# Kernel optimization log

Measured on AMD Instinct MI355X. Metric: run time of the kernel, lower is better.

Reference implementation:

```python
import math
import jax, jax.numpy as jnp
import numpy as np

# CoordinateDescentRouter defaults (lucidrains/CoLT5-attention)
N_ITERS, EPS, EPS_INIT, EPS_DECAY, FETCH_K_RATIO = 20, 0.03, 4.0, 0.7, 9.0 / 8.0

B, N, D, G, H, DH, NQ, NKV = 2, 4096, 1024, 2, 16, 64, 1024, 1024
DIM_INNER = H * DH  # 1024


def coor_descent(s, k):
    # s: (b, g, n). Differentiable top-k relaxation via coordinate descent.
    logk = math.log(k)
    eps_sched = [max(EPS_INIT * EPS_DECAY ** i, EPS) for i in range(N_ITERS + 1)]
    b = -s
    a = jnp.zeros_like(s[..., :1])
    for ce in eps_sched[:-1]:
        sb = (s + b) / ce
        a = ce * (logk - jax.scipy.special.logsumexp(sb, axis=-1, keepdims=True))
        b = -jax.nn.relu(s + a)
    return jnp.exp((s + a + b) / eps_sched[-1])


def route(x, routing_tokens, num_tokens):
    # x: (b,n,d), routing_tokens: (g,d) -> indices (b,g,nt), scores (b,g,nt), routed (b,g,nt,d)
    bsz, n, _ = x.shape
    k_cd = min(int(num_tokens * FETCH_K_RATIO), n)
    sim = jnp.einsum('bnd,gd->bgn', x, routing_tokens)
    scores = coor_descent(sim, k_cd)
    scores, idx = jax.lax.top_k(scores, num_tokens)
    # straight-through: forward value 1.0, gradient flows through coor_descent scores
    scores = scores + jax.lax.stop_gradient(1.0 - scores)
    routed = x[jnp.arange(bsz)[:, None, None], idx]
    return idx, scores, routed


def rmsnorm(t, gamma):
    # t: (b,g,n,d); F.normalize over feature dim * sqrt(d) * gamma (g,d)
    norm = jnp.sqrt(jnp.sum(t * t, axis=-1, keepdims=True))
    return t / jnp.maximum(norm, 1e-12) * math.sqrt(t.shape[-1]) * gamma[None, :, None, :]


def grouped_attention(queries, kvs, v_scale, o_scale, gamma_q, gamma_c, wq, wkv, wo, null_kv):
    bsz, g, nq, d = queries.shape
    h, dh = null_kv.shape[2], null_kv.shape[-1]
    qn = rmsnorm(queries, gamma_q)
    cn = rmsnorm(kvs, gamma_c)
    # grouped 1x1 conv == per-group linear; within-group output channel order is (h, dh)
    q = jnp.einsum('bgnd,ged->bgne', qn, wq)
    kv = jnp.einsum('bgnd,ged->bgne', cn, wkv)
    k, v = jnp.split(kv, 2, axis=-1)

    def to_heads(t):
        return t.reshape(bsz, g, t.shape[2], h, dh).transpose(0, 1, 3, 2, 4)  # (b,g,h,n,dh)

    q, k, v = map(to_heads, (q, k, v))
    v = v * v_scale  # (b,g,1,nkv,1) broadcast, applied before null kv concat
    nk = jnp.broadcast_to(null_kv[0][None], (bsz,) + null_kv[0].shape)
    nv = jnp.broadcast_to(null_kv[1][None], (bsz,) + null_kv[1].shape)
    k = jnp.concatenate([nk, k], axis=-2)
    v = jnp.concatenate([nv, v], axis=-2)
    sim = jnp.einsum('bghnd,bghmd->bghnm', q * dh ** -0.5, k)
    attn = jax.nn.softmax(sim, axis=-1)
    o = jnp.einsum('bghnm,bghmd->bghnd', attn, v)
    o = o.transpose(0, 1, 3, 2, 4).reshape(bsz, g, nq, h * dh)
    o = jnp.einsum('bgne,gde->bgnd', o, wo)
    return o * o_scale


def setup_inputs() -> dict:
    key = jax.random.key(0)
    ks = jax.random.split(key, 8)
    inv = 1.0 / math.sqrt(D)
    return {
        'x': jax.random.normal(ks[0], (B, N, D), jnp.float32),
        'rt_q': jax.random.normal(ks[1], (G, D), jnp.float32),
        'rt_kv': jax.random.normal(ks[2], (G, D), jnp.float32),
        'gamma_q': jnp.ones((G, D), jnp.float32),
        'gamma_c': jnp.ones((G, D), jnp.float32),
        'wq': jax.random.normal(ks[3], (G, DIM_INNER, D), jnp.float32) * inv,
        'wkv': jax.random.normal(ks[4], (G, 2 * DIM_INNER, D), jnp.float32) * inv,
        'wo': jax.random.normal(ks[5], (G, D, DIM_INNER), jnp.float32) * inv,
        'null_kv': jax.random.normal(ks[6], (2, G, H, 1, DH), jnp.float32),
        'null_token': jax.random.normal(ks[7], (1, 1, D), jnp.float32),
        'num_routed_queries': NQ,
        'num_routed_key_values': NKV,
    }


def reference(x, rt_q, rt_kv, gamma_q, gamma_c, wq, wkv, wo, null_kv, null_token,
              num_routed_queries, num_routed_key_values):
    bsz, n, d = x.shape
    q_idx, q_scores, queries = route(x, rt_q, num_routed_queries)
    _, kv_scores, key_values = route(x, rt_kv, num_routed_key_values)
    v_scale = kv_scores[:, :, None, :, None]  # (b,g,1,nkv,1)
    o_scale = q_scores[..., None]             # (b,g,nq,1)
    attn_out = grouped_attention(queries, key_values, v_scale, o_scale,
                                 gamma_q, gamma_c, wq, wkv, wo, null_kv)
    # scatter routed outputs back, averaging over experts that picked each token
    flat_idx = q_idx.reshape(bsz, -1)                 # (b, g*nq)
    flat_out = attn_out.reshape(bsz, -1, d)           # (b, g*nq, d)
    bidx = jnp.arange(bsz)[:, None]
    summed = jnp.zeros_like(x).at[bidx, flat_idx].add(flat_out)
    counts = jnp.zeros((bsz, n), x.dtype).at[bidx, flat_idx].add(1.0)
    not_routed = (counts == 0.0)[..., None]
    summed = jnp.where(not_routed, 0.0, summed)
    out = summed / jnp.maximum(counts[..., None], 1e-5)
    out = jnp.where(not_routed, null_token, out)
    return out
```

## Files before the change

### kernel.cpp

```cpp
#include <hip/hip_runtime.h>

typedef __attribute__((ext_vector_type(8))) short short8;
typedef __attribute__((ext_vector_type(4))) short short4v;
typedef __attribute__((ext_vector_type(4))) float f32x4;

#define B_ 2
#define N_ 4096
#define D_ 1024
#define G_ 2
#define H_ 16
#define DH_ 64
#define NSLOT 1088
#define LOGK 7.0492548412558374f
#define ATTN_SCALE 0.18033688011112043f
#define FIXED_M 32.0f

#define BAR() __builtin_amdgcn_s_barrier()
#define WAITV4 asm volatile("s_waitcnt vmcnt(4)" ::: "memory")
#define WAITV0 asm volatile("s_waitcnt vmcnt(0)" ::: "memory")
#define GLDS(src, dst) __builtin_amdgcn_global_load_lds( \
    (const __attribute__((address_space(1))) void*)(src), \
    (__attribute__((address_space(3))) void*)(dst), 16, 0, 0)

__device__ __forceinline__ float bf2f(short s) {
  return __uint_as_float(((unsigned)(unsigned short)s) << 16);
}
__device__ __forceinline__ short f2bf(float f) {
  unsigned u = __float_as_uint(f);
  u = (u + 0x7FFFu + ((u >> 16) & 1u)) >> 16;
  return (short)u;
}
__device__ __forceinline__ short f2bf_trunc(float f) {
  return (short)(__float_as_uint(f) >> 16);
}

__global__ __launch_bounds__(256) void prep_kernel(
    const float* __restrict__ wq, const float* __restrict__ wkv,
    const float* __restrict__ wo, short* __restrict__ dq,
    short* __restrict__ dkv, short* __restrict__ dwo,
    const float* __restrict__ x, const float* __restrict__ rtq,
    const float* __restrict__ rtkv, float* __restrict__ sim,
    const float* __restrict__ null_kv, short* __restrict__ kb_,
    short* __restrict__ vb_)
{
  int bid = blockIdx.x;
  if (bid < 8192) {
    int i = bid * 256 + threadIdx.x;
    const float* src; short* dst;
    if (i < 524288) { src = wq; dst = dq; }
    else if (i < 1572864) { src = wkv; dst = dkv; i -= 524288; }
    else { src = wo; dst = dwo; i -= 1572864; }
    f32x4 v = ((const f32x4*)src)[i];
    short4v o;
#pragma unroll
    for (int e = 0; e < 4; ++e) o[e] = f2bf(v[e]);
    ((short4v*)dst)[i] = o;
  } else if (bid < 10240) {
    int wid = threadIdx.x >> 6, lane = threadIdx.x & 63;
    int row = (bid - 8192) * 4 + wid;
    int b = row >> 12, n = row & (N_ - 1);
    const float* xr = x + (size_t)row * D_;
    float a0 = 0.f, a1 = 0.f, a2 = 0.f, a3 = 0.f;
#pragma unroll
    for (int c = 0; c < 4; ++c) {
      int d = c * 256 + lane * 4;
      f32x4 xv = *(const f32x4*)(xr + d);
      f32x4 r0 = *(const f32x4*)(rtq + d);
      f32x4 r1 = *(const f32x4*)(rtq + D_ + d);
      f32x4 r2 = *(const f32x4*)(rtkv + d);
      f32x4 r3 = *(const f32x4*)(rtkv + D_ + d);
#pragma unroll
      for (int e = 0; e < 4; ++e) {
        a0 += xv[e] * r0[e];
        a1 += xv[e] * r1[e];
        a2 += xv[e] * r2[e];
        a3 += xv[e] * r3[e];
      }
    }
#pragma unroll
    for (int o = 32; o; o >>= 1) {
      a0 += __shfl_xor(a0, o); a1 += __shfl_xor(a1, o);
      a2 += __shfl_xor(a2, o); a3 += __shfl_xor(a3, o);
    }
    if (lane == 0) {
      sim[((size_t)(b)*G_ + 0) * N_ + n] = a0;
      sim[((size_t)(b)*G_ + 1) * N_ + n] = a1;
      sim[((size_t)(B_ + b)*G_ + 0) * N_ + n] = a2;
      sim[((size_t)(B_ + b)*G_ + 1) * N_ + n] = a3;
    }
  } else {
    int bgh = (bid - 10240) * 4 + (threadIdx.x >> 6);
    int g = (bgh >> 4) & 1, h = bgh & 15;
    int t = threadIdx.x & 63;
    float kvk = null_kv[((size_t)(0 * G_ + g) * H_ + h) * DH_ + t];
    float kvv = null_kv[((size_t)(1 * G_ + g) * H_ + h) * DH_ + t];
    kb_[((size_t)bgh * NSLOT + 1024) * DH_ + t] = f2bf(kvk);
    vb_[((size_t)bgh * DH_ + t) * NSLOT + 1024] = f2bf(kvv);
  }
}

__global__ __launch_bounds__(1024) void coor_topk(
    const float* __restrict__ sim, int* __restrict__ idxout, int* __restrict__ inv)
{
  __shared__ float rbuf[16];
  __shared__ float res;
  __shared__ unsigned keys[N_];
  __shared__ int scanbuf[16];

  int r = blockIdx.x >> 2, b = (blockIdx.x >> 1) & 1, g = blockIdx.x & 1;
  const float* srow = sim + ((size_t)blockIdx.x << 12);
  int tid = threadIdx.x, lane = tid & 63, wid = tid >> 6;

  float sv[4];
#pragma unroll
  for (int j = 0; j < 4; ++j) sv[j] = srow[tid * 4 + j];

  float a = 0.f;
  double epsd = 4.0;
  for (int it = 0; it < 20; ++it) {
    float eps = (float)fmax(epsd, 0.03);
    epsd *= 0.7;
    float sb[4]; float lmax = -INFINITY;
#pragma unroll
    for (int j = 0; j < 4; ++j) {
      float bb = (it == 0) ? (-sv[j]) : (-fmaxf(sv[j] + a, 0.f));
      sb[j] = (sv[j] + bb) / eps;
      lmax = fmaxf(lmax, sb[j]);
    }
#pragma unroll
    for (int o = 32; o; o >>= 1) lmax = fmaxf(lmax, __shfl_xor(lmax, o));
    if (lane == 0) rbuf[wid] = lmax;
    __syncthreads();
    if (tid < 64) {
      float m = (tid < 16) ? rbuf[tid] : -INFINITY;
#pragma unroll
      for (int o = 8; o; o >>= 1) m = fmaxf(m, __shfl_xor(m, o));
      if (tid == 0) res = m;
    }
    __syncthreads();
    float mx = res;
    float lsum = 0.f;
#pragma unroll
    for (int j = 0; j < 4; ++j) lsum += expf(sb[j] - mx);
#pragma unroll
    for (int o = 32; o; o >>= 1) lsum += __shfl_xor(lsum, o);
    if (lane == 0) rbuf[wid] = lsum;
    __syncthreads();
    if (tid < 64) {
      float s = (tid < 16) ? rbuf[tid] : 0.f;
#pragma unroll
      for (int o = 8; o; o >>= 1) s += __shfl_xor(s, o);
      if (tid == 0) res = logf(s) + mx;
    }
    __syncthreads();
    float lse = res;
    a = eps * (LOGK - lse);
  }
  __syncthreads();

  unsigned kb[4]; int c1 = 0;
#pragma unroll
  for (int j = 0; j < 4; ++j) {
    float sc = expf(fminf(sv[j] + a, 0.f) / 0.03f);
    kb[j] = __float_as_uint(sc);
    keys[tid * 4 + j] = kb[j];
    c1 += (kb[j] == 0x3F800000u);
  }
#pragma unroll
  for (int o = 32; o; o >>= 1) c1 += __shfl_xor(c1, o);
  if (lane == 0) scanbuf[wid] = c1;
  __syncthreads();
  int c1tot = 0;
  for (int i = 0; i < 16; ++i) c1tot += scanbuf[i];
  __syncthreads();

  int flag[4];
  if (c1tot >= 1024) {
#pragma unroll
    for (int j = 0; j < 4; ++j) flag[j] = (kb[j] == 0x3F800000u);
  } else {
#pragma unroll
    for (int j = 0; j < 4; ++j) {
      unsigned kn = kb[j]; int n = tid * 4 + j; int rank = 0;
      for (int m = 0; m < N_; ++m) {
        unsigned km = keys[m];
        rank += (km > kn) || (km == kn && m < n);
      }
      flag[j] = (rank < 1024);
    }
  }

  int cnt = flag[0] + flag[1] + flag[2] + flag[3];
  int inc = cnt;
#pragma unroll
  for (int o = 1; o < 64; o <<= 1) {
    int tt = __shfl_up(inc, o);
    if (lane >= o) inc += tt;
  }
  if (lane == 63) scanbuf[wid] = inc;
  __syncthreads();
  int off = 0;
  for (int w = 0; w < wid; ++w) off += scanbuf[w];
  int pos = off + inc - cnt;
  int* op = idxout + ((size_t)blockIdx.x << 10);
  int* ip = inv + ((size_t)(b * G_ + g) << 12);
#pragma unroll
  for (int j = 0; j < 4; ++j) {
    if (flag[j]) {
      if (pos < 1024) {
        int n = tid * 4 + j;
        op[pos] = n;
        if (r == 0) ip[n] = pos;
      }
      pos++;
    }
  }
}

__global__ __launch_bounds__(256) void gather_rms(
    const float* __restrict__ x, const int* __restrict__ idx,
    const float* __restrict__ gamma_q, const float* __restrict__ gamma_c,
    short* __restrict__ qn, short* __restrict__ cn)
{
  __shared__ float rb[4];
  __shared__ float tot;
  int id = blockIdx.x;
  int r = id >> 12, rem = id & 4095;
  int g = (rem >> 10) & 1;
  int b = rem >> 11;
  int tok = idx[id];
  int t = threadIdx.x;
  const float* xr = x + ((size_t)b * N_ + tok) * D_;
  f32x4 v = *(const f32x4*)(xr + t * 4);
  float ss = v[0]*v[0] + v[1]*v[1] + v[2]*v[2] + v[3]*v[3];
#pragma unroll
  for (int o = 32; o; o >>= 1) ss += __shfl_xor(ss, o);
  if ((t & 63) == 0) rb[t >> 6] = ss;
  __syncthreads();
  if (t == 0) tot = rb[0] + rb[1] + rb[2] + rb[3];
  __syncthreads();
  float scale = 32.0f / fmaxf(sqrtf(tot), 1e-12f);
  const float* gm = (r ? gamma_c : gamma_q) + g * D_;
  f32x4 gv = *(const f32x4*)(gm + t * 4);
  short* dst = (r ? cn : qn) + ((size_t)rem << 10) + t * 4;
  short4v ov;
#pragma unroll
  for (int e = 0; e < 4; ++e) ov[e] = f2bf(v[e] * scale * gv[e]);
  *(short4v*)dst = ov;
}

__global__ __launch_bounds__(256, 3) void gemm_qkv(
    const short* __restrict__ qn, const short* __restrict__ cn,
    const short* __restrict__ wqb, const short* __restrict__ wkvb,
    short* __restrict__ qout, short* __restrict__ kout, short* __restrict__ vout)
{
  __shared__ short As[8192];
  __shared__ short Bs[8192];
  int t = threadIdx.x, lane = t & 63, wid = t >> 6;
  int grp = lane >> 4, l15 = lane & 15;
  int wm = wid >> 1, wn = wid & 1;
  int lin = blockIdx.x + 8 * (blockIdx.y + 24 * blockIdx.z);
  int s = (lin & 7) * 96 + (lin >> 3);
  int bx = s & 7, ny = (s >> 3) % 24, bg = s / 192;
  bool isq = ny < 8;
  const short* A  = isq ? qn : cn;
  const short* Bw = isq ? wqb : wkvb;
  int NB = isq ? 1024 : 2048;
  int nbase = (isq ? ny : ny - 8) * 128;
  float oscale = isq ? ATTN_SCALE : 1.0f;
  int mbase = bx * 128;
  int g = bg & 1;
  const short* Ab = A + ((size_t)bg << 20);
  const short* Bp = Bw + ((size_t)g * NB + nbase) * 1024;

  f32x4 zero = {0.f, 0.f, 0.f, 0.f};
  f32x4 acc[4][4];
#pragma unroll
  for (int i = 0; i < 4; ++i)
#pragma unroll
    for (int j = 0; j < 4; ++j) acc[i][j] = zero;

  const short* apA[4]; const short* apB[4]; int dstoff[4];
#pragma unroll
  for (int c = 0; c < 4; ++c) {
    int u = c * 256 + t;
    int row = u >> 3, j = u & 7;
    int cu = (j ^ (row & 7)) << 3;
    apA[c] = Ab + ((size_t)(mbase + row) << 10) + cu;
    apB[c] = Bp + ((size_t)row << 10) + cu;
    dstoff[c] = c * 2048 + wid * 512;
  }

  for (int kb = 0; kb < 16; ++kb) {
    int ko = kb * 64;
    if (kb) __syncthreads();
#pragma unroll
    for (int c = 0; c < 4; ++c) {
      GLDS(apA[c] + ko, As + dstoff[c]);
      GLDS(apB[c] + ko, Bs + dstoff[c]);
    }
    WAITV0;
    __syncthreads();
    const char* Ac = (const char*)As;
    const char* Bc = (const char*)Bs;
#pragma unroll
    for (int kf = 0; kf < 2; ++kf) {
      short8 af[4], bf_[4];
#pragma unroll
      for (int mt = 0; mt < 4; ++mt) {
        int ra = wm * 64 + mt * 16 + l15;
        af[mt] = *(const short8*)(Ac + ra * 128 + (((grp << 4) + (kf << 6)) ^ ((ra & 7) << 4)));
      }
#pragma unroll
      for (int nt = 0; nt < 4; ++nt) {
        int rb = wn * 64 + nt * 16 + l15;
        bf_[nt] = *(const short8*)(Bc + rb * 128 + (((grp << 4) + (kf << 6)) ^ ((rb & 7) << 4)));
      }
      __builtin_amdgcn_s_setprio(1);
#pragma unroll
      for (int mt = 0; mt < 4; ++mt)
#pragma unroll
        for (int nt = 0; nt < 4; ++nt)
          acc[mt][nt] = __builtin_amdgcn_mfma_f32_16x16x32_bf16(af[mt], bf_[nt], acc[mt][nt], 0, 0, 0);
      __builtin_amdgcn_s_setprio(0);
    }
  }

#pragma unroll
  for (int mt = 0; mt < 4; ++mt)
#pragma unroll
    for (int nt = 0; nt < 4; ++nt) {
      int n = nbase + wn*64 + nt*16 + l15;
#pragma unroll
      for (int rr = 0; rr < 4; ++rr) {
        int m = mbase + wm*64 + mt*16 + grp*4 + rr;
        float v = acc[mt][nt][rr] * oscale;
        if (isq) {
          qout[((size_t)bg * 1024 + m) * 1024 + n] = f2bf(v);
        } else {
          if (n < 1024) {
            kout[(((size_t)bg * H_ + (n >> 6)) * NSLOT + m) * DH_ + (n & 63)] = f2bf(v);
          } else {
            int e = n - 1024;
            vout[(((size_t)bg * H_ + (e >> 6)) * DH_ + (e & 63)) * NSLOT + m] = f2bf(v);
          }
        }
      }
    }
}

__global__ __launch_bounds__(256, 3) void gemm_wo(
    const short* __restrict__ A, const short* __restrict__ Bw,
    short* __restrict__ out0, short* __restrict__ out1)
{
  __shared__ short As[8192];
  __shared__ short Bs[8192];
  int t = threadIdx.x, lane = t & 63, wid = t >> 6;
  int grp = lane >> 4, l15 = lane & 15;
  int wm = wid >> 1, wn = wid & 1;
  int lin = blockIdx.x + 8 * (blockIdx.y + 8 * blockIdx.z);
  int s = (lin & 7) * 64 + (lin >> 3);
  int mbase = (s & 7) * 128, nbase = ((s >> 3) & 7) * 128;
  int z = s >> 6, bg = z >> 1, sp = z & 1, g = bg & 1;
  short* out = sp ? out1 : out0;
  const short* Ab = A + ((size_t)bg << 20);
  const short* Bp = Bw + ((size_t)g * 1024 + nbase) * 1024;

  f32x4 zero = {0.f, 0.f, 0.f, 0.f};
  f32x4 acc[4][4];
#pragma unroll
  for (int i = 0; i < 4; ++i)
#pragma unroll
    for (int j = 0; j < 4; ++j) acc[i][j] = zero;

  const short* apA[4]; const short* apB[4]; int dstoff[4];
#pragma unroll
  for (int c = 0; c < 4; ++c) {
    int u = c * 256 + t;
    int row = u >> 3, j = u & 7;
    int cu = (j ^ (row & 7)) << 3;
    apA[c] = Ab + ((size_t)(mbase + row) << 10) + cu;
    apB[c] = Bp + ((size_t)row << 10) + cu;
    dstoff[c] = c * 2048 + wid * 512;
  }

  int kb0 = sp * 8;
  for (int kk = 0; kk < 8; ++kk) {
    int ko = (kb0 + kk) * 64;
    if (kk) __syncthreads();
#pragma unroll
    for (int c = 0; c < 4; ++c) {
      GLDS(apA[c] + ko, As + dstoff[c]);
      GLDS(apB[c] + ko, Bs + dstoff[c]);
    }
    WAITV0;
    __syncthreads();
    const char* Ac = (const char*)As;
    const char* Bc = (const char*)Bs;
#pragma unroll
    for (int kf = 0; kf < 2; ++kf) {
      short8 af[4], bf_[4];
#pragma unroll
      for (int mt = 0; mt < 4; ++mt) {
        int ra = wm * 64 + mt * 16 + l15;
        af[mt] = *(const short8*)(Ac + ra * 128 + (((grp << 4) + (kf << 6)) ^ ((ra & 7) << 4)));
      }
#pragma unroll
      for (int nt = 0; nt < 4; ++nt) {
        int rb = wn * 64 + nt * 16 + l15;
        bf_[nt] = *(const short8*)(Bc + rb * 128 + (((grp << 4) + (kf << 6)) ^ ((rb & 7) << 4)));
      }
      __builtin_amdgcn_s_setprio(1);
#pragma unroll
      for (int mt = 0; mt < 4; ++mt)
#pragma unroll
        for (int nt = 0; nt < 4; ++nt)
          acc[mt][nt] = __builtin_amdgcn_mfma_f32_16x16x32_bf16(af[mt], bf_[nt], acc[mt][nt], 0, 0, 0);
      __builtin_amdgcn_s_setprio(0);
    }
  }

#pragma unroll
  for (int mt = 0; mt < 4; ++mt)
#pragma unroll
    for (int nt = 0; nt < 4; ++nt) {
      int n = nbase + wn*64 + nt*16 + l15;
#pragma unroll
      for (int rr = 0; rr < 4; ++rr) {
        int m = mbase + wm*64 + mt*16 + grp*4 + rr;
        out[((size_t)bg * 1024 + m) * 1024 + n] = f2bf(acc[mt][nt][rr]);
      }
    }
}

__global__ __launch_bounds__(256, 3) void attn_kernel(
    const short* __restrict__ q, const short* __restrict__ k,
    const short* __restrict__ vT, short* __restrict__ o0,
    short* __restrict__ o1, float* __restrict__ ml)
{
  __shared__ short Ks[2][4096];
  __shared__ short Vs[2][4096];
  __shared__ short Ps[4][32 * 72];
  int bgh = blockIdx.x, qb = blockIdx.y, sp = blockIdx.z;
  int bg = bgh >> 4, h = bgh & 15;
  int wid = threadIdx.x >> 6, lane = threadIdx.x & 63;
  int l15 = lane & 15, grp = lane >> 4;
  int qbase = qb * 128 + wid * 32;
  short* Pw = &Ps[wid][0];

  short8 bq[2][2];
#pragma unroll
  for (int qh = 0; qh < 2; ++qh) {
    const short* qp = q + ((size_t)bg * 1024 + qbase + qh * 16 + l15) * 1024 + h * 64 + (grp << 3);
    bq[qh][0] = *(const short8*)qp;
    bq[qh][1] = *(const short8*)(qp + 32);
  }
  short8 ones8;
  short ov = (l15 == 0) ? (short)0x3F80 : (short)0;
#pragma unroll
  for (int e = 0; e < 8; ++e) ones8[e] = ov;

  int u0 = wid * 128 + lane, u1 = u0 + 64;
  int r0 = u0 >> 3, j0 = u0 & 7, r1 = u1 >> 3, j1 = u1 & 7;
  const short* kbase = k + (size_t)bgh * NSLOT * DH_;
  const short* vbase = vT + (size_t)bgh * DH_ * NSLOT;
  const short* kss0 = kbase + r0 * 64 + ((j0 ^ (r0 & 7)) << 3);
  const short* kss1 = kbase + r1 * 64 + ((j1 ^ (r1 & 7)) << 3);
  const short* vss0 = vbase + (size_t)r0 * NSLOT + ((j0 ^ (r0 & 7)) << 3);
  const short* vss1 = vbase + (size_t)r1 * NSLOT + ((j1 ^ (r1 & 7)) << 3);

  f32x4 zero = {0.f, 0.f, 0.f, 0.f};
  f32x4 minit = {-FIXED_M, -FIXED_M, -FIXED_M, -FIXED_M};
  f32x4 oacc[2][4], lacc[2];
#pragma unroll
  for (int qh = 0; qh < 2; ++qh) {
    lacc[qh] = zero;
#pragma unroll
    for (int dt = 0; dt < 4; ++dt) oacc[qh][dt] = zero;
  }

  auto STAGE = [&](int tile, int p) {
    size_t ko = (size_t)tile * 4096;
    size_t vo = (size_t)tile * 64;
    short* kd = &Ks[p][0] + wid * 1024;
    short* vd = &Vs[p][0] + wid * 1024;
    GLDS(kss0 + ko, kd);
    GLDS(kss1 + ko, kd + 512);
    GLDS(vss0 + vo, vd);
    GLDS(vss1 + vo, vd + 512);
  };

  auto PROCESS = [&](int tile, int p) {
    const char* Kc = (const char*)&Ks[p][0];
    const char* Vc = (const char*)&Vs[p][0];
    f32x4 sacc[2][4];
#pragma unroll
    for (int qh = 0; qh < 2; ++qh)
#pragma unroll
      for (int kt = 0; kt < 4; ++kt) sacc[qh][kt] = minit;
#pragma unroll
    for (int kf = 0; kf < 2; ++kf) {
      short8 ka[4];
#pragma unroll
      for (int kt = 0; kt < 4; ++kt) {
        int ra = kt * 16 + l15;
        ka[kt] = *(const short8*)(Kc + ra * 128 + (((grp + 4 * kf) ^ (ra & 7)) << 4));
      }
      __builtin_amdgcn_s_setprio(1);
#pragma unroll
      for (int kt = 0; kt < 4; ++kt)
#pragma unroll
        for (int qh = 0; qh < 2; ++qh)
          sacc[qh][kt] = __builtin_amdgcn_mfma_f32_16x16x32_bf16(ka[kt], bq[qh][kf], sacc[qh][kt], 0, 0, 0);
      __builtin_amdgcn_s_setprio(0);
    }
    if (tile == 16) {
#pragma unroll
      for (int qh = 0; qh < 2; ++qh)
#pragma unroll
        for (int kt = 0; kt < 4; ++kt)
#pragma unroll
          for (int rr = 0; rr < 4; ++rr)
            if ((kt * 16 + (grp << 2) + rr) != 0) sacc[qh][kt][rr] = -INFINITY;
    }
#pragma unroll
    for (int qh = 0; qh < 2; ++qh)
#pragma unroll
      for (int kt = 0; kt < 4; ++kt) {
        short4v pk;
#pragma unroll
        for (int rr = 0; rr < 4; ++rr) pk[rr] = f2bf_trunc(exp2f(sacc[qh][kt][rr]));
        *(short4v*)(Pw + (qh * 16 + l15) * 72 + kt * 16 + (grp << 2)) = pk;
      }
#pragma unroll
    for (int ks = 0; ks < 2; ++ks) {
      short8 pa[2];
#pragma unroll
      for (int qh = 0; qh < 2; ++qh)
        pa[qh] = *(const short8*)((const char*)Pw + (qh * 16 + l15) * 144 + grp * 16 + ks * 64);
      __builtin_amdgcn_s_setprio(1);
#pragma unroll
      for (int dt = 0; dt < 4; ++dt) {
        int ra = dt * 16 + l15;
        short8 vbf = *(const short8*)(Vc + ra * 128 + (((grp + 4 * ks) ^ (ra & 7)) << 4));
#pragma unroll
        for (int qh = 0; qh < 2; ++qh)
          oacc[qh][dt] = __builtin_amdgcn_mfma_f32_16x16x32_bf16(pa[qh], vbf, oacc[qh][dt], 0, 0, 0);
      }
#pragma unroll
      for (int qh = 0; qh < 2; ++qh)
        lacc[qh] = __builtin_amdgcn_mfma_f32_16x16x32_bf16(pa[qh], ones8, lacc[qh], 0, 0, 0);
      __builtin_amdgcn_s_setprio(0);
    }
  };

  int t0 = sp ? 8 : 0, t1 = sp ? 17 : 8;
  STAGE(t0, 0);
  STAGE(t0 + 1, 1);
  WAITV4;
  BAR();
  for (int tile = t0; tile < t1; ++tile) {
    int p = (tile - t0) & 1;
    PROCESS(tile, p);
    if (tile + 1 < t1) {
      BAR();
      if (tile + 2 < t1) { STAGE(tile + 2, p); WAITV4; }
      else               { WAITV0; }
      BAR();
    }
  }

  if (l15 == 0) {
#pragma unroll
    for (int qh = 0; qh < 2; ++qh)
#pragma unroll
      for (int rr = 0; rr < 4; ++rr)
        ml[(size_t)(sp * 64 + bgh) * 1024 + qbase + qh * 16 + (grp << 2) + rr] = lacc[qh][rr];
  }
#pragma unroll
  for (int qh = 0; qh < 2; ++qh)
#pragma unroll
    for (int dt = 0; dt < 4; ++dt)
#pragma unroll
      for (int rr = 0; rr < 4; ++rr) {
        int qq = qh * 16 + (grp << 2) + rr;
        int dh = dt * 16 + l15;
        if (sp == 0)
          o0[((size_t)bg * 1024 + qbase + qq) * 1024 + h * 64 + dh] = f2bf(oacc[qh][dt][rr]);
        else
          o1[((size_t)bgh * 1024 + qbase + qq) * 64 + dh] = f2bf(oacc[qh][dt][rr]);
      }
}

__global__ __launch_bounds__(256) void attn_merge(
    short* __restrict__ obuf, const short* __restrict__ op1,
    const float* __restrict__ ml)
{
  int id = blockIdx.x;
  int bgh = id >> 4, qc = id & 15;
  int bg = bgh >> 4, h = bgh & 15;
  int t = threadIdx.x;
  int qq = t >> 2, c = t & 3;
  int qrow = qc * 64 + qq;
  float l0 = ml[(size_t)bgh * 1024 + qrow];
  float l1 = ml[(size_t)(64 + bgh) * 1024 + qrow];
  float w = 1.0f / (l0 + l1);
  size_t loc0 = ((size_t)bg * 1024 + qrow) * 1024 + h * 64 + c * 16;
  size_t loc1 = ((size_t)bgh * 1024 + qrow) * 64 + c * 16;
  short8 a0 = *(const short8*)(obuf + loc0);
  short8 a1 = *(const short8*)(obuf + loc0 + 8);
  short8 b0 = *(const short8*)(op1 + loc1);
  short8 b1 = *(const short8*)(op1 + loc1 + 8);
  short8 r0, r1;
#pragma unroll
  for (int e = 0; e < 8; ++e) {
    r0[e] = f2bf((bf2f(a0[e]) + bf2f(b0[e])) * w);
    r1[e] = f2bf((bf2f(a1[e]) + bf2f(b1[e])) * w);
  }
  *(short8*)(obuf + loc0) = r0;
  *(short8*)(obuf + loc0 + 8) = r1;
}

__global__ __launch_bounds__(256) void finalize_kernel(
    const short* __restrict__ wo0, const short* __restrict__ wo1,
    const int* __restrict__ inv, const float* __restrict__ null_token,
    float* __restrict__ outp)
{
  int id = blockIdx.x;
  int b = id >> 12, n = id & (N_ - 1);
  int s0 = inv[((size_t)(b * G_ + 0) << 12) + n];
  int s1 = inv[((size_t)(b * G_ + 1) << 12) + n];
  int t = threadIdx.x;
  float* dst = outp + (size_t)id * D_ + t * 4;
  if (s0 < 0 && s1 < 0) {
    *(f32x4*)dst = *(const f32x4*)(null_token + t * 4);
  } else {
    f32x4 sum = {0.f, 0.f, 0.f, 0.f};
    float cnt = 0.f;
    if (s0 >= 0) {
      size_t loc = (((size_t)(b * G_ + 0) * 1024 + s0) << 10) + t * 4;
      short4v v = *(const short4v*)(wo0 + loc);
      short4v v2 = *(const short4v*)(wo1 + loc);
#pragma unroll
      for (int e = 0; e < 4; ++e) sum[e] += bf2f(v[e]) + bf2f(v2[e]);
      cnt += 1.f;
    }
    if (s1 >= 0) {
      size_t loc = (((size_t)(b * G_ + 1) * 1024 + s1) << 10) + t * 4;
      short4v v = *(const short4v*)(wo0 + loc);
      short4v v2 = *(const short4v*)(wo1 + loc);
#pragma unroll
      for (int e = 0; e < 4; ++e) sum[e] += bf2f(v[e]) + bf2f(v2[e]);
      cnt += 1.f;
    }
    f32x4 rv;
#pragma unroll
    for (int e = 0; e < 4; ++e) rv[e] = sum[e] / cnt;
    *(f32x4*)dst = rv;
  }
}

extern "C" void kernel_launch(void* const* d_in, const int* in_sizes, int n_in,
                              void* d_out, int out_size, void* d_ws, size_t ws_size,
                              hipStream_t stream) {
  (void)in_sizes; (void)n_in; (void)out_size; (void)ws_size;
  const float* x        = (const float*)d_in[0];
  const float* rt_q     = (const float*)d_in[1];
  const float* rt_kv    = (const float*)d_in[2];
  const float* gamma_q  = (const float*)d_in[3];
  const float* gamma_c  = (const float*)d_in[4];
  const float* wq       = (const float*)d_in[5];
  const float* wkv      = (const float*)d_in[6];
  const float* wo       = (const float*)d_in[7];
  const float* null_kv  = (const float*)d_in[8];
  const float* null_tok = (const float*)d_in[9];
  float* outp = (float*)d_out;

  char* ws = (char*)d_ws;
  size_t off = 0;
  auto alloc = [&](size_t bytes) { char* p = ws + off; off += (bytes + 255) & ~(size_t)255; return p; };
  float* sim   = (float*)alloc((size_t)2 * B_ * G_ * N_ * 4);
  int*   idx   = (int*)  alloc((size_t)2 * B_ * G_ * 1024 * 4);
  int*   inv   = (int*)  alloc((size_t)B_ * G_ * N_ * 4);
  float* ml    = (float*)alloc((size_t)2 * 64 * 1024 * 4);
  short* qn    = (short*)alloc((size_t)B_ * G_ * 1024 * 1024 * 2);
  short* cn    = (short*)alloc((size_t)B_ * G_ * 1024 * 1024 * 2);
  short* qproj = (short*)alloc((size_t)B_ * G_ * 1024 * 1024 * 2);
  size_t kvbytes = (size_t)B_ * G_ * H_ * NSLOT * DH_ * 2;
  short* kbuf  = (short*)alloc(kvbytes);
  short* vbuf  = (short*)alloc(kvbytes);
  short* obuf  = (short*)alloc((size_t)B_ * G_ * 1024 * 1024 * 2);
  short* wobuf = (short*)alloc((size_t)B_ * G_ * 1024 * 1024 * 2);
  short* wo_bf = (short*)alloc((size_t)G_ * 1024 * 1024 * 2);
  short* wq_bf  = wobuf;
  short* wkv_bf = obuf;
  short* op1    = cn;
  short* wobuf2 = qproj;

  hipMemsetAsync(inv, 0xFF, (size_t)B_ * G_ * N_ * 4, stream);

  prep_kernel<<<10256, 256, 0, stream>>>(wq, wkv, wo, wq_bf, wkv_bf, wo_bf,
                                         x, rt_q, rt_kv, sim, null_kv, kbuf, vbuf);
  coor_topk<<<8, 1024, 0, stream>>>(sim, idx, inv);
  gather_rms<<<2 * B_ * G_ * 1024, 256, 0, stream>>>(x, idx, gamma_q, gamma_c, qn, cn);
  gemm_qkv<<<dim3(8, 24, B_ * G_), 256, 0, stream>>>(qn, cn, wq_bf, wkv_bf, qproj, kbuf, vbuf);
  attn_kernel<<<dim3(64, 8, 2), 256, 0, stream>>>(qproj, kbuf, vbuf, obuf, op1, ml);
  attn_merge<<<1024, 256, 0, stream>>>(obuf, op1, ml);
  gemm_wo<<<dim3(8, 8, 2 * B_ * G_), 256, 0, stream>>>(obuf, wo_bf, wobuf, wobuf2);
  finalize_kernel<<<B_ * N_, 256, 0, stream>>>(wobuf, wobuf2, inv, null_tok, outp);
}
```

Baseline: 169.7 us.

## Overlap weight bf16 conversion with top-k kernel and merge softmax reductions

Moves the fp32-to-bf16 weight conversion out of the prep kernel and into extra blocks of the coordinate-descent top-k kernel. The 8 serial top-k blocks then share the GPU with conversion work instead of running nearly alone. It also merges the max and sum reductions in each coordinate-descent iteration into one online log-sum-exp pass, removing two block barriers per iteration. The risks are that the 1024-thread conversion blocks may be scheduled ahead of the top-k blocks, and that the top-k blocks' large shared allocation now also applies to conversion blocks, which can limit occupancy.

```diff
diff --git a/kernel.cpp b/kernel.cpp
--- a/kernel.cpp
+++ b/kernel.cpp
@@ -35,29 +35,15 @@
 }
 
 __global__ __launch_bounds__(256) void prep_kernel(
-    const float* __restrict__ wq, const float* __restrict__ wkv,
-    const float* __restrict__ wo, short* __restrict__ dq,
-    short* __restrict__ dkv, short* __restrict__ dwo,
     const float* __restrict__ x, const float* __restrict__ rtq,
     const float* __restrict__ rtkv, float* __restrict__ sim,
     const float* __restrict__ null_kv, short* __restrict__ kb_,
     short* __restrict__ vb_)
 {
   int bid = blockIdx.x;
-  if (bid < 8192) {
-    int i = bid * 256 + threadIdx.x;
-    const float* src; short* dst;
-    if (i < 524288) { src = wq; dst = dq; }
-    else if (i < 1572864) { src = wkv; dst = dkv; i -= 524288; }
-    else { src = wo; dst = dwo; i -= 1572864; }
-    f32x4 v = ((const f32x4*)src)[i];
-    short4v o;
-#pragma unroll
-    for (int e = 0; e < 4; ++e) o[e] = f2bf(v[e]);
-    ((short4v*)dst)[i] = o;
-  } else if (bid < 10240) {
+  if (bid < 2048) {
     int wid = threadIdx.x >> 6, lane = threadIdx.x & 63;
-    int row = (bid - 8192) * 4 + wid;
+    int row = bid * 4 + wid;
     int b = row >> 12, n = row & (N_ - 1);
     const float* xr = x + (size_t)row * D_;
     float a0 = 0.f, a1 = 0.f, a2 = 0.f, a3 = 0.f;
@@ -89,7 +75,7 @@
       sim[((size_t)(B_ + b)*G_ + 1) * N_ + n] = a3;
     }
   } else {
-    int bgh = (bid - 10240) * 4 + (threadIdx.x >> 6);
+    int bgh = (bid - 2048) * 4 + (threadIdx.x >> 6);
     int g = (bgh >> 4) & 1, h = bgh & 15;
     int t = threadIdx.x & 63;
     float kvk = null_kv[((size_t)(0 * G_ + g) * H_ + h) * DH_ + t];
@@ -99,10 +85,32 @@
   }
 }
 
-__global__ __launch_bounds__(1024) void coor_topk(
-    const float* __restrict__ sim, int* __restrict__ idxout, int* __restrict__ inv)
+__global__ __launch_bounds__(1024) void topk_wconv(
+    const float* __restrict__ sim, int* __restrict__ idxout, int* __restrict__ inv,
+    const float* __restrict__ wq, const float* __restrict__ wkv,
+    const float* __restrict__ wo, short* __restrict__ dq,
+    short* __restrict__ dkv, short* __restrict__ dwo)
 {
-  __shared__ float rbuf[16];
+  if (blockIdx.x >= 8) {
+    int base = (blockIdx.x - 8) * 4096 + threadIdx.x;
+#pragma unroll
+    for (int c = 0; c < 4; ++c) {
+      int i = base + c * 1024;
+      const float* src; short* dst;
+      if (i < 524288) { src = wq; dst = dq; }
+      else if (i < 1572864) { src = wkv; dst = dkv; i -= 524288; }
+      else { src = wo; dst = dwo; i -= 1572864; }
+      f32x4 v = ((const f32x4*)src)[i];
+      short4v o;
+#pragma unroll
+      for (int e = 0; e < 4; ++e) o[e] = f2bf(v[e]);
+      ((short4v*)dst)[i] = o;
+    }
+    return;
+  }
+
+  __shared__ float rbm[16];
+  __shared__ float rbs[16];
   __shared__ float res;
   __shared__ unsigned keys[N_];
   __shared__ int scanbuf[16];
@@ -120,37 +128,33 @@
   for (int it = 0; it < 20; ++it) {
     float eps = (float)fmax(epsd, 0.03);
     epsd *= 0.7;
-    float sb[4]; float lmax = -INFINITY;
+    float sb[4]; float mt = -INFINITY;
 #pragma unroll
     for (int j = 0; j < 4; ++j) {
       float bb = (it == 0) ? (-sv[j]) : (-fmaxf(sv[j] + a, 0.f));
       sb[j] = (sv[j] + bb) / eps;
-      lmax = fmaxf(lmax, sb[j]);
-    }
-#pragma unroll
-    for (int o = 32; o; o >>= 1) lmax = fmaxf(lmax, __shfl_xor(lmax, o));
-    if (lane == 0) rbuf[wid] = lmax;
+      mt = fmaxf(mt, sb[j]);
+    }
+#pragma unroll
+    for (int o = 32; o; o >>= 1) mt = fmaxf(mt, __shfl_xor(mt, o));
+    float st = 0.f;
+#pragma unroll
+    for (int j = 0; j < 4; ++j) st += expf(sb[j] - mt);
+#pragma unroll
+    for (int o = 32; o; o >>= 1) st += __shfl_xor(st, o);
+    if (lane == 0) { rbm[wid] = mt; rbs[wid] = st; }
     __syncthreads();
     if (tid < 64) {
-      float m = (tid < 16) ? rbuf[tid] : -INFINITY;
-#pragma unroll
-      for (int o = 8; o; o >>= 1) m = fmaxf(m, __shfl_xor(m, o));
-      if (tid == 0) res = m;
-    }
-    __syncthreads();
-    float mx = res;
-    float lsum = 0.f;
-#pragma unroll
-    for (int j = 0; j < 4; ++j) lsum += expf(sb[j] - mx);
-#pragma unroll
-    for (int o = 32; o; o >>= 1) lsum += __shfl_xor(lsum, o);
-    if (lane == 0) rbuf[wid] = lsum;
-    __syncthreads();
-    if (tid < 64) {
-      float s = (tid < 16) ? rbuf[tid] : 0.f;
-#pragma unroll
-      for (int o = 8; o; o >>= 1) s += __shfl_xor(s, o);
-      if (tid == 0) res = logf(s) + mx;
+      float m2 = (tid < 16) ? rbm[tid] : -INFINITY;
+      float s2 = (tid < 16) ? rbs[tid] : 0.f;
+#pragma unroll
+      for (int o = 8; o; o >>= 1) {
+        float mo = __shfl_xor(m2, o), so = __shfl_xor(s2, o);
+        float mn = fmaxf(m2, mo);
+        s2 = s2 * expf(m2 - mn) + so * expf(mo - mn);
+        m2 = mn;
+      }
+      if (tid == 0) res = logf(s2) + m2;
     }
     __syncthreads();
     float lse = res;
@@ -699,9 +703,9 @@
 
   hipMemsetAsync(inv, 0xFF, (size_t)B_ * G_ * N_ * 4, stream);
 
-  prep_kernel<<<10256, 256, 0, stream>>>(wq, wkv, wo, wq_bf, wkv_bf, wo_bf,
-                                         x, rt_q, rt_kv, sim, null_kv, kbuf, vbuf);
-  coor_topk<<<8, 1024, 0, stream>>>(sim, idx, inv);
+  prep_kernel<<<2064, 256, 0, stream>>>(x, rt_q, rt_kv, sim, null_kv, kbuf, vbuf);
+  topk_wconv<<<520, 1024, 0, stream>>>(sim, idx, inv, wq, wkv, wo,
+                                       wq_bf, wkv_bf, wo_bf);
   gather_rms<<<2 * B_ * G_ * 1024, 256, 0, stream>>>(x, idx, gamma_q, gamma_c, qn, cn);
   gemm_qkv<<<dim3(8, 24, B_ * G_), 256, 0, stream>>>(qn, cn, wq_bf, wkv_bf, qproj, kbuf, vbuf);
   attn_kernel<<<dim3(64, 8, 2), 256, 0, stream>>>(qproj, kbuf, vbuf, obuf, op1, ml);
```

New measurement: 164.9 us. 1.03x faster.
